# Performance work log

Measured on AMD Instinct MI355X. Metric: run time of the kernel, lower is better.

The kernel has to match this reference:

```python
import jax, jax.numpy as jnp
import numpy as np

C, Q, R, N, S = 10, 1000, 1024, 512, 10000
ALPHA, GAMMA, DIST_W, EPS_EYE = 0.25, 2.0, 0.1, 1e-4


def setup_inputs() -> dict:
    key = jax.random.key(0)
    ks = jax.random.split(key, 8)
    box_features = jax.random.normal(ks[0], (N, R), jnp.float32)
    id_labels = jax.random.randint(ks[1], (N,), 0, C, dtype=jnp.int32)
    id_data = jax.random.normal(ks[2], (C, Q, R), jnp.float32)
    id_data_counter = jnp.full((C,), Q, dtype=jnp.int32)  # full queues -> VOS path enabled
    W_pred = jax.random.normal(ks[3], (C, R), jnp.float32) * 0.02
    b_pred = jnp.zeros((C,), jnp.float32)
    w_e = jax.random.uniform(ks[4], (C, 1), jnp.float32)  # energy_score_weights ~ U[0,1)
    dist_W1 = jax.random.normal(ks[5], (512, 1), jnp.float32) * 0.5
    dist_b1 = jnp.zeros((512,), jnp.float32)
    dist_W2 = jax.random.normal(ks[6], (1, 512), jnp.float32) * 0.05
    dist_b2 = jnp.zeros((1,), jnp.float32)
    eps = jax.random.normal(ks[7], (C, S, R), jnp.float32)  # standard-normal draws for rsample
    return dict(box_features=box_features, id_labels=id_labels, id_data=id_data,
                id_data_counter=id_data_counter, W_pred=W_pred, b_pred=b_pred, w_e=w_e,
                dist_W1=dist_W1, dist_b1=dist_b1, dist_W2=dist_W2, dist_b2=dist_b2, eps=eps)


def _bce_logits(x, y):
    # binary_cross_entropy_with_logits, elementwise
    return jnp.maximum(x, 0.0) - x * y + jnp.log1p(jnp.exp(-jnp.abs(x)))


def _queue_update(id_data, counter, labels, feats):
    # Faithful sequential per-sample queue scatter (torch Python loop) as lax.scan.
    def step(carry, inp):
        data, cnt = carry
        lab, f = inp
        c = cnt[lab]
        row = data[lab]                                            # [Q,R]
        row_set = jax.lax.dynamic_update_slice(row, f[None], (c, 0))
        row_roll = jnp.concatenate([row[1:], f[None]], axis=0)     # drop oldest, append
        full = c >= row.shape[0]
        new_row = jnp.where(full, row_roll, row_set)
        data = data.at[lab].set(new_row)
        cnt = cnt.at[lab].add(jnp.where(full, 0, 1))
        return (data, cnt), None
    (data, cnt), _ = jax.lax.scan(step, (id_data, counter), (labels, feats))
    return data, cnt


def _energy(x, w_e):
    # m + log(exp(x-m) @ relu(w_e)); all classes valid (counter > 0)
    m = jnp.max(x, axis=1, keepdims=True)
    return m + jnp.log(jnp.exp(x - m) @ jax.nn.relu(w_e))


def reference(box_features, id_labels, id_data, id_data_counter, W_pred, b_pred, w_e,
              dist_W1, dist_b1, dist_W2, dist_b2, eps):
    scores = box_features @ W_pred.T + b_pred                      # [N,C]
    # ---- classification: sigmoid focal loss (sum / num_pos) ----
    t = jax.nn.one_hot(id_labels, C, dtype=scores.dtype)
    p = jax.nn.sigmoid(scores)
    ce = _bce_logits(scores, t)
    p_t = p * t + (1.0 - p) * (1.0 - t)
    alpha_t = ALPHA * t + (1.0 - ALPHA) * (1.0 - t)
    cls_loss = jnp.sum(alpha_t * ce * (1.0 - p_t) ** GAMMA) / scores.shape[0]
    # ---- per-class queue scatter (detached features) ----
    data, _ = _queue_update(id_data, id_data_counter, id_labels,
                            jax.lax.stop_gradient(box_features))
    # ---- class Gaussians: per-class mean, shared covariance ----
    mu = jnp.mean(data, axis=1)                                    # [C,R]
    x_tilda = (data - mu[:, None, :]).reshape(-1, R)               # all classes valid (full queues)
    sigma = x_tilda.T @ x_tilda / x_tilda.shape[0] + EPS_EYE * jnp.eye(R, dtype=data.dtype)
    L = jnp.linalg.cholesky(sigma)                                 # [R,R]
    # ---- VOS: rsample 10000 per class, keep lowest-density (top-1 of -log_prob) ----
    # samples = mu + eps @ L.T ; log_prob = const - 0.5*||eps||^2, so argmin density = argmax ||eps||^2
    sq = jnp.sum(eps * eps, axis=-1)                               # [C,S]
    idx = jnp.argmax(sq, axis=-1)                                  # [C]
    eps_sel = jnp.take_along_axis(eps, idx[:, None, None], axis=1)[:, 0, :]  # [C,R]
    vos_samples = mu + eps_sel @ L.T                               # [C,R]
    scores_vos = vos_samples @ W_pred.T + b_pred                   # [C,C]
    # ---- dist loss: energy score -> tiny MLP -> BCE, weight 0.1 ----
    e_all = jnp.concatenate([_energy(scores, w_e), _energy(scores_vos, w_e)], axis=0)  # [N+C,1]
    h = jax.nn.relu(e_all @ dist_W1.T + dist_b1)
    logits = (h @ dist_W2.T + dist_b2)[:, 0]                       # [N+C]
    y = jnp.concatenate([jnp.ones((scores.shape[0],), logits.dtype),
                         jnp.zeros((C,), logits.dtype)])
    dist_loss = DIST_W * jnp.mean(_bce_logits(logits, y))
    return cls_loss, dist_loss
```

## Files before the change

kernel.cpp:

```cpp
#include <hip/hip_runtime.h>
#include <stdint.h>

#define C_ 10
#define Q_ 1000
#define R_ 1024
#define N_ 512
#define S_ 10000
#define CQ 10000
#define KP 10240

#define OFF_DT    0ULL
#define OFF_GP    20971520ULL
#define OFF_SIG   37748736ULL
#define OFF_MU    41943040ULL
#define OFF_E     41984000ULL
#define OFF_CLS   41986088ULL
#define OFF_AMAX  41986096ULL
#define OFF_KC    41986176ULL
#define OFF_GOFF  41986216ULL
#define OFF_GIDX  41986256ULL

typedef __attribute__((ext_vector_type(8))) short bf16x8;
typedef __attribute__((ext_vector_type(4))) float f32x4;

__global__ void k_prep(const int* __restrict__ labels, int* kc, int* goff, int* gidx,
                       float* mu, float* cls_accum, unsigned long long* amax) {
  __shared__ int cnt[C_];
  __shared__ int off[C_];
  int t = threadIdx.x;
  if (t < C_) cnt[t] = 0;
  __syncthreads();
  for (int i = t; i < N_; i += 256) atomicAdd(&cnt[labels[i]], 1);
  __syncthreads();
  if (t == 0) {
    int acc = 0;
    for (int c = 0; c < C_; c++) { off[c] = acc; goff[c] = acc; kc[c] = cnt[c]; acc += cnt[c]; }
    for (int i = 0; i < N_; i++) { int c = labels[i]; gidx[off[c]++] = i; }
    *cls_accum = 0.f;
  }
  if (t < C_) amax[t] = 0ULL;
  for (int i = t; i < C_ * R_; i += 256) mu[i] = 0.f;
}

__global__ __launch_bounds__(256) void k_epsmax(const float* __restrict__ eps,
                                                unsigned long long* amax) {
  int c = blockIdx.y;
  int chunk = blockIdx.x;
  int t = threadIdx.x, lane = t & 63, w = t >> 6;
  const int per = 79;
  int s0 = chunk * per;
  int s1 = min(s0 + per, S_);
  float bv = -1.f; int bs = 0;
  for (int s = s0 + w; s < s1; s += 4) {
    const float4* p = (const float4*)(eps + ((size_t)c * S_ + s) * R_);
    float acc = 0.f;
#pragma unroll
    for (int m = 0; m < 4; m++) {
      float4 v = p[lane + 64 * m];
      acc += v.x * v.x + v.y * v.y + v.z * v.z + v.w * v.w;
    }
#pragma unroll
    for (int d = 32; d > 0; d >>= 1) acc += __shfl_xor(acc, d);
    if (acc > bv) { bv = acc; bs = s; }
  }
  __shared__ float svv[4]; __shared__ int ssi[4];
  if (lane == 0) { svv[w] = bv; ssi[w] = bs; }
  __syncthreads();
  if (t == 0) {
    float m = svv[0]; int mi = ssi[0];
    for (int i = 1; i < 4; i++) if (svv[i] > m) { m = svv[i]; mi = ssi[i]; }
    if (m >= 0.f) {
      unsigned long long pk = ((unsigned long long)__float_as_uint(m) << 32) | (unsigned)mi;
      atomicMax(amax + c, pk);
    }
  }
}

__global__ void k_scores(const float* __restrict__ box, const int* __restrict__ labels,
                         const float* __restrict__ Wp, const float* __restrict__ bp,
                         const float* __restrict__ we, float* __restrict__ E,
                         float* cls_accum) {
  int i = blockIdx.x;
  int lane = threadIdx.x;
  float s[C_];
#pragma unroll
  for (int k = 0; k < C_; k++) s[k] = 0.f;
  const float* bi = box + (size_t)i * R_;
  for (int r = lane; r < R_; r += 64) {
    float x = bi[r];
#pragma unroll
    for (int k = 0; k < C_; k++) s[k] += x * Wp[k * R_ + r];
  }
#pragma unroll
  for (int k = 0; k < C_; k++) {
#pragma unroll
    for (int d = 32; d > 0; d >>= 1) s[k] += __shfl_xor(s[k], d);
  }
  if (lane == 0) {
    int lab = labels[i];
    float sc[C_]; float m = -1e30f;
#pragma unroll
    for (int k = 0; k < C_; k++) { sc[k] = s[k] + bp[k]; m = fmaxf(m, sc[k]); }
    float fsum = 0.f, esum = 0.f;
#pragma unroll
    for (int k = 0; k < C_; k++) {
      float x = sc[k];
      float tt = (k == lab) ? 1.f : 0.f;
      float p = 1.f / (1.f + expf(-x));
      float ce = fmaxf(x, 0.f) - x * tt + log1pf(expf(-fabsf(x)));
      float pt = p * tt + (1.f - p) * (1.f - tt);
      float at = 0.25f * tt + 0.75f * (1.f - tt);
      float om = 1.f - pt;
      fsum += at * ce * om * om;
      esum += expf(x - m) * fmaxf(we[k], 0.f);
    }
    atomicAdd(cls_accum, fsum);
    E[i] = m + logf(esum);
  }
}

__global__ __launch_bounds__(256) void k_convert(const float* __restrict__ idd,
                                                 const float* __restrict__ box,
                                                 const int* __restrict__ kc,
                                                 const int* __restrict__ goff,
                                                 const int* __restrict__ gidx,
                                                 uint16_t* __restrict__ Dt,
                                                 float* __restrict__ mu) {
  __shared__ const float* rowsrc[64];
  __shared__ int rcls[64];
  __shared__ float T[64][65];
  int bk = blockIdx.x;
  int br = blockIdx.y;
  int t = threadIdx.x;
  int t0 = bk * 64, r0 = br * 64;
  if (t < 64) {
    int row = t0 + t;
    const float* src = nullptr; int c = -1;
    if (row < CQ) {
      c = row / Q_;
      int q = row - c * Q_;
      int k = kc[c];
      if (q < Q_ - k) src = idd + (size_t)(c * Q_ + q + k) * R_;
      else            src = box + (size_t)gidx[goff[c] + (q - (Q_ - k))] * R_;
    }
    rowsrc[t] = src; rcls[t] = c;
  }
  __syncthreads();
  int rr = t & 63, k4 = t >> 6;
#pragma unroll
  for (int it = 0; it < 16; it++) {
    int kk = k4 + it * 4;
    const float* src = rowsrc[kk];
    T[kk][rr] = src ? src[r0 + rr] : 0.f;
  }
  __syncthreads();
  if (t < 64 && t0 < CQ) {
    int c0 = rcls[0];
    float s0 = 0.f, s1 = 0.f; int c1 = -1;
    for (int kk = 0; kk < 64; kk++) {
      int c = rcls[kk]; float v = T[kk][t];
      if (c == c0) s0 += v; else if (c >= 0) { c1 = c; s1 += v; }
    }
    atomicAdd(&mu[c0 * R_ + r0 + t], s0);
    if (c1 >= 0) atomicAdd(&mu[c1 * R_ + r0 + t], s1);
  }
  int kk2 = t & 63, r4 = t >> 6;
#pragma unroll
  for (int it = 0; it < 16; it++) {
    int rr2 = r4 + it * 4;
    float v = T[kk2][rr2];
    uint32_t u = __float_as_uint(v);
    uint32_t b = (u + 0x7fffu + ((u >> 16) & 1u)) >> 16;
    Dt[(size_t)(r0 + rr2) * KP + t0 + kk2] = (uint16_t)b;
  }
}

__global__ __launch_bounds__(256) void k_gemm(const uint16_t* __restrict__ Dt,
                                              float* __restrict__ GP) {
  __shared__ uint16_t lA[128 * 64];
  __shared__ uint16_t lB[128 * 64];
  int bi = blockIdx.x, bj = blockIdx.y, bz = blockIdx.z;
  int t = threadIdx.x;
  int lane = t & 63, w = t >> 6;
  int i0 = bi * 128, j0 = bj * 128;
  int lane16 = lane & 15, quad = lane >> 4;
  int wm = w >> 1, wn = w & 1;
  int srow = t >> 1, shalf = t & 1;
  const uint4* DU = (const uint4*)Dt;
  int kz0 = bz * 320;
  f32x4 acc[4][4];
#pragma unroll
  for (int a = 0; a < 4; a++)
#pragma unroll
    for (int b = 0; b < 4; b++) acc[a][b] = (f32x4){0.f, 0.f, 0.f, 0.f};

  for (int kt8 = 0; kt8 < 320; kt8 += 8) {
    const uint4* pa = DU + (size_t)(i0 + srow) * 1280 + kz0 + kt8 + shalf * 4;
    const uint4* pb = DU + (size_t)(j0 + srow) * 1280 + kz0 + kt8 + shalf * 4;
    uint4* la4 = (uint4*)(lA + srow * 64 + shalf * 32);
    uint4* lb4 = (uint4*)(lB + srow * 64 + shalf * 32);
#pragma unroll
    for (int u = 0; u < 4; u++) la4[u] = pa[u];
#pragma unroll
    for (int u = 0; u < 4; u++) lb4[u] = pb[u];
    __syncthreads();
#pragma unroll
    for (int ch = 0; ch < 2; ch++) {
      bf16x8 af[4], bfr[4];
#pragma unroll
      for (int mi = 0; mi < 4; mi++)
        af[mi] = *(const bf16x8*)(lA + (wm * 64 + mi * 16 + lane16) * 64 + ch * 32 + quad * 8);
#pragma unroll
      for (int ni = 0; ni < 4; ni++)
        bfr[ni] = *(const bf16x8*)(lB + (wn * 64 + ni * 16 + lane16) * 64 + ch * 32 + quad * 8);
#pragma unroll
      for (int mi = 0; mi < 4; mi++)
#pragma unroll
        for (int ni = 0; ni < 4; ni++)
          acc[mi][ni] = __builtin_amdgcn_mfma_f32_16x16x32_bf16(af[mi], bfr[ni], acc[mi][ni], 0, 0, 0);
    }
    __syncthreads();
  }
  float* gp = GP + (size_t)bz * 1048576;
#pragma unroll
  for (int mi = 0; mi < 4; mi++)
#pragma unroll
    for (int ni = 0; ni < 4; ni++) {
      int col = j0 + wn * 64 + ni * 16 + lane16;
      int rowb = i0 + wm * 64 + mi * 16 + quad * 4;
#pragma unroll
      for (int r = 0; r < 4; r++)
        gp[(size_t)(rowb + r) * 1024 + col] = acc[mi][ni][r];
    }
}

__global__ void k_reduce(const float* __restrict__ GP, const float* __restrict__ mu,
                         float* __restrict__ sig) {
  int idx = blockIdx.x * 256 + threadIdx.x;
  int i = idx >> 10, j = idx & 1023;
  float g = GP[idx] + GP[idx + 1048576] + GP[idx + 2097152] + GP[idx + 3145728];
  float mm = 0.f;
#pragma unroll
  for (int c = 0; c < C_; c++) mm += mu[c * R_ + i] * mu[c * R_ + j];
  sig[idx] = g * 1e-4f - mm * 1e-7f + ((i == j) ? 1e-4f : 0.f);
}

#define AIDX(i, j) (((i) << 7) + (((j) + (i)) & 127))
__global__ __launch_bounds__(256) void k_chol_diag(float* __restrict__ sig, int p) {
  __shared__ float a[16384];
  int t = threadIdx.x;
  int base = p * 128;
  int lane = t & 63, wv = t >> 6;
  for (int idx = t; idx < 16384; idx += 256) {
    int i = idx >> 7, j = idx & 127;
    a[AIDX(i, j)] = sig[(size_t)(base + i) * 1024 + base + j];
  }
  __syncthreads();
  for (int panel = 0; panel < 8; panel++) {
    int j0 = panel * 16;
    if (wv == 0) {
      float pa0[16], pa1[16];
#pragma unroll
      for (int jj = 0; jj < 16; jj++) {
        pa0[jj] = a[AIDX(lane, j0 + jj)];
        pa1[jj] = a[AIDX(lane + 64, j0 + jj)];
      }
#pragma unroll
      for (int jj = 0; jj < 16; jj++) {
        int j = j0 + jj;
        float pv0 = __shfl(pa0[jj], j & 63);
        float pv1 = __shfl(pa1[jj], j & 63);
        float pv = (j < 64) ? pv0 : pv1;
        float rsq = rsqrtf(pv);
        rsq = rsq * (1.5f - 0.5f * pv * rsq * rsq);
        pa0[jj] *= rsq;
        pa1[jj] *= rsq;
#pragma unroll
        for (int kk = jj + 1; kk < 16; kk++) {
          int k = j0 + kk;
          float av0 = __shfl(pa0[jj], k & 63);
          float av1 = __shfl(pa1[jj], k & 63);
          float akj = (k < 64) ? av0 : av1;
          pa0[kk] -= pa0[jj] * akj;
          pa1[kk] -= pa1[jj] * akj;
        }
      }
#pragma unroll
      for (int jj = 0; jj < 16; jj++) {
        a[AIDX(lane, j0 + jj)] = pa0[jj];
        a[AIDX(lane + 64, j0 + jj)] = pa1[jj];
      }
    }
    __syncthreads();
    int m0 = j0 + 16;
    int M = 128 - m0;
    if (M > 0) {
      int T4 = M >> 2;
      int ntiles = T4 * (T4 + 1) / 2;
      for (int tb = t; tb < ntiles; tb += 256) {
        int I = (int)((sqrtf(8.f * tb + 1.f) - 1.f) * 0.5f);
        while ((I + 1) * (I + 2) / 2 <= tb) I++;
        while (I * (I + 1) / 2 > tb) I--;
        int K = tb - I * (I + 1) / 2;
        int gi = m0 + I * 4, gk = m0 + K * 4;
        float acc[4][4] = {{0.f}};
#pragma unroll
        for (int u = 0; u < 16; u++) {
          int jj = (u + t) & 15;
          float ai[4], ak[4];
#pragma unroll
          for (int m = 0; m < 4; m++) ai[m] = a[AIDX(gi + m, j0 + jj)];
#pragma unroll
          for (int n = 0; n < 4; n++) ak[n] = a[AIDX(gk + n, j0 + jj)];
#pragma unroll
          for (int m = 0; m < 4; m++)
#pragma unroll
            for (int n = 0; n < 4; n++) acc[m][n] += ai[m] * ak[n];
        }
#pragma unroll
        for (int m = 0; m < 4; m++)
#pragma unroll
          for (int n = 0; n < 4; n++)
            a[AIDX(gi + m, gk + n)] -= acc[m][n];
      }
    }
    __syncthreads();
  }
  for (int idx = t; idx < 16384; idx += 256) {
    int i = idx >> 7, j = idx & 127;
    sig[(size_t)(base + i) * 1024 + base + j] = a[AIDX(i, j)];
  }
}

#define XIDX(j, r) (((j) << 6) + (((r) + (j)) & 63))
__global__ __launch_bounds__(256) void k_chol_trsm(float* __restrict__ sig, int p) {
  __shared__ float Ls[8128];
  __shared__ float XT[8192];
  int t = threadIdx.x;
  int base = p * 128;
  int row0 = base + 128 + blockIdx.x * 64;
  int r = t & 63, wv = t >> 6;
  for (int idx = t; idx < 8128; idx += 256) {
    int k = (int)((sqrtf(8.f * idx + 1.f) + 1.f) * 0.5f);
    while (k * (k - 1) / 2 > idx) k--;
    while ((k + 1) * k / 2 <= idx) k++;
    int j = idx - k * (k - 1) / 2;
    Ls[idx] = sig[(size_t)(base + k) * 1024 + base + j];
  }
  for (int idx = t; idx < 8192; idx += 256) {
    int rr = idx >> 7, j = idx & 127;
    XT[XIDX(j, rr)] = sig[(size_t)(row0 + rr) * 1024 + base + j];
  }
  float rd0 = 0.f, rd1 = 0.f;
  if (wv == 0) {
    rd0 = 1.0f / sig[(size_t)(base + r) * 1024 + base + r];
    rd1 = 1.0f / sig[(size_t)(base + 64 + r) * 1024 + base + 64 + r];
  }
  __syncthreads();
  for (int pb = 0; pb < 8; pb++) {
    int j0 = pb * 16;
    if (j0 > 0) {
      int c0 = j0 + wv * 4;
      int b0 = c0 * (c0 - 1) / 2, b1 = (c0 + 1) * c0 / 2;
      int b2 = (c0 + 2) * (c0 + 1) / 2, b3 = (c0 + 3) * (c0 + 2) / 2;
      float acc0 = 0.f, acc1 = 0.f, acc2 = 0.f, acc3 = 0.f;
      for (int k = 0; k < j0; k++) {
        float xk = XT[XIDX(k, r)];
        acc0 += xk * Ls[b0 + k];
        acc1 += xk * Ls[b1 + k];
        acc2 += xk * Ls[b2 + k];
        acc3 += xk * Ls[b3 + k];
      }
      XT[XIDX(c0 + 0, r)] -= acc0;
      XT[XIDX(c0 + 1, r)] -= acc1;
      XT[XIDX(c0 + 2, r)] -= acc2;
      XT[XIDX(c0 + 3, r)] -= acc3;
    }
    __syncthreads();
    if (wv == 0) {
#pragma unroll
      for (int jj = 0; jj < 16; jj++) {
        int j = j0 + jj;
        float rdj = (j < 64) ? __shfl(rd0, j & 63) : __shfl(rd1, j & 63);
        float xj = XT[XIDX(j, r)] * rdj;
        XT[XIDX(j, r)] = xj;
#pragma unroll
        for (int kk = jj + 1; kk < 16; kk++) {
          int k2 = j0 + kk;
          XT[XIDX(k2, r)] -= xj * Ls[k2 * (k2 - 1) / 2 + j];
        }
      }
    }
    __syncthreads();
  }
  for (int idx = t; idx < 8192; idx += 256) {
    int rr = idx >> 7, j = idx & 127;
    sig[(size_t)(row0 + rr) * 1024 + base + j] = XT[XIDX(j, rr)];
  }
}

__global__ __launch_bounds__(256) void k_chol_syrk(float* __restrict__ sig, int p) {
  __shared__ float PA[64][65], PB[64][65];
  int t = threadIdx.x;
  int tb = p * 128 + 128;
  int bx = blockIdx.x;
  int I = 0;
  while ((I + 1) * (I + 2) / 2 <= bx) I++;
  int K = bx - I * (I + 1) / 2;
  int gi = tb + I * 64, gk = tb + K * 64;
  int a4 = t >> 4, b4 = t & 15;
  float acc[4][4];
#pragma unroll
  for (int m = 0; m < 4; m++)
#pragma unroll
    for (int n = 0; n < 4; n++) acc[m][n] = 0.f;
  for (int ch = 0; ch < 2; ch++) {
    int cb = p * 128 + ch * 64;
    for (int idx = t; idx < 4096; idx += 256) {
      int rr = idx >> 6, cc = idx & 63;
      PA[rr][cc] = sig[(size_t)(gi + rr) * 1024 + cb + cc];
      PB[rr][cc] = sig[(size_t)(gk + rr) * 1024 + cb + cc];
    }
    __syncthreads();
    for (int j = 0; j < 64; j++) {
      float pa[4], pb[4];
#pragma unroll
      for (int m = 0; m < 4; m++) pa[m] = PA[a4 * 4 + m][j];
#pragma unroll
      for (int n = 0; n < 4; n++) pb[n] = PB[b4 * 4 + n][j];
#pragma unroll
      for (int m = 0; m < 4; m++)
#pragma unroll
        for (int n = 0; n < 4; n++) acc[m][n] += pa[m] * pb[n];
    }
    __syncthreads();
  }
#pragma unroll
  for (int m = 0; m < 4; m++)
#pragma unroll
    for (int n = 0; n < 4; n++)
      sig[(size_t)(gi + a4 * 4 + m) * 1024 + gk + b4 * 4 + n] -= acc[m][n];
}

__global__ __launch_bounds__(256) void k_vos(const float* __restrict__ eps,
                                             const float* __restrict__ L,
                                             const float* __restrict__ mu,
                                             const float* __restrict__ Wp,
                                             const float* __restrict__ bp,
                                             const float* __restrict__ we,
                                             const unsigned long long* __restrict__ amax,
                                             float* __restrict__ E) {
  __shared__ float es[1024];
  __shared__ float ys[1024];
  __shared__ float sv[16];
  int c = blockIdx.x, t = threadIdx.x;
  int idx = (int)(amax[c] & 0xffffffffULL);
  for (int i = t; i < 1024; i += 256) es[i] = eps[((size_t)c * S_ + idx) * R_ + i];
  __syncthreads();
  for (int rep = 0; rep < 4; rep++) {
    int i = rep * 256 + t;
    const float* Lr = L + (size_t)i * 1024;
    float a0 = 0.f, a1 = 0.f, a2 = 0.f, a3 = 0.f;
    int j = 0;
    for (; j + 3 <= i; j += 4) {
      a0 += es[j] * Lr[j];
      a1 += es[j + 1] * Lr[j + 1];
      a2 += es[j + 2] * Lr[j + 2];
      a3 += es[j + 3] * Lr[j + 3];
    }
    for (; j <= i; j++) a0 += es[j] * Lr[j];
    ys[i] = mu[c * R_ + i] * 1e-3f + ((a0 + a1) + (a2 + a3));
  }
  __syncthreads();
  if (t < C_) {
    float acc = bp[t];
    const float* Wr = Wp + (size_t)t * R_;
    for (int j = 0; j < 1024; j++) acc += ys[j] * Wr[j];
    sv[t] = acc;
  }
  __syncthreads();
  if (t == 0) {
    float m = -1e30f;
    for (int k = 0; k < C_; k++) m = fmaxf(m, sv[k]);
    float sum = 0.f;
    for (int k = 0; k < C_; k++) sum += expf(sv[k] - m) * fmaxf(we[k], 0.f);
    E[N_ + c] = m + logf(sum);
  }
}

__global__ __launch_bounds__(256) void k_dist(const float* __restrict__ E,
                                              const float* __restrict__ W1,
                                              const float* __restrict__ b1,
                                              const float* __restrict__ W2,
                                              const float* __restrict__ b2,
                                              const float* __restrict__ cls_accum,
                                              float* __restrict__ out) {
  __shared__ float sW1[512], sb1[512], sW2[512];
  __shared__ float red[4];
  int t = threadIdx.x;
  for (int i = t; i < 512; i += 256) { sW1[i] = W1[i]; sb1[i] = b1[i]; sW2[i] = W2[i]; }
  __syncthreads();
  float sum = 0.f;
  for (int i = t; i < N_ + C_; i += 256) {
    float e = E[i];
    float acc = b2[0];
    for (int j = 0; j < 512; j++) acc += sW2[j] * fmaxf(e * sW1[j] + sb1[j], 0.f);
    float y = (i < N_) ? 1.f : 0.f;
    float l = fmaxf(acc, 0.f) - acc * y + log1pf(expf(-fabsf(acc)));
    sum += l;
  }
#pragma unroll
  for (int d = 32; d > 0; d >>= 1) sum += __shfl_xor(sum, d);
  if ((t & 63) == 0) red[t >> 6] = sum;
  __syncthreads();
  if (t == 0) {
    out[1] = 0.1f * (red[0] + red[1] + red[2] + red[3]) / 522.f;
    out[0] = *cls_accum / 512.f;
  }
}

extern "C" void kernel_launch(void* const* d_in, const int* in_sizes, int n_in,
                              void* d_out, int out_size, void* d_ws, size_t ws_size,
                              hipStream_t stream) {
  (void)in_sizes; (void)n_in; (void)out_size; (void)ws_size;
  const float* box  = (const float*)d_in[0];
  const int*   lab  = (const int*)d_in[1];
  const float* idd  = (const float*)d_in[2];
  const float* Wp   = (const float*)d_in[4];
  const float* bp   = (const float*)d_in[5];
  const float* we   = (const float*)d_in[6];
  const float* W1   = (const float*)d_in[7];
  const float* b1   = (const float*)d_in[8];
  const float* W2   = (const float*)d_in[9];
  const float* b2   = (const float*)d_in[10];
  const float* eps  = (const float*)d_in[11];
  float* out = (float*)d_out;

  char* ws = (char*)d_ws;
  uint16_t* Dt = (uint16_t*)(ws + OFF_DT);
  float* GP    = (float*)(ws + OFF_GP);
  float* sig   = (float*)(ws + OFF_SIG);
  float* mu    = (float*)(ws + OFF_MU);
  float* E     = (float*)(ws + OFF_E);
  float* clsa  = (float*)(ws + OFF_CLS);
  unsigned long long* amax = (unsigned long long*)(ws + OFF_AMAX);
  int* kc   = (int*)(ws + OFF_KC);
  int* goff = (int*)(ws + OFF_GOFF);
  int* gidx = (int*)(ws + OFF_GIDX);

  hipLaunchKernelGGL(k_prep, dim3(1), dim3(256), 0, stream, lab, kc, goff, gidx, mu, clsa, amax);
  hipLaunchKernelGGL(k_epsmax, dim3(127, C_), dim3(256), 0, stream, eps, amax);
  hipLaunchKernelGGL(k_scores, dim3(N_), dim3(64), 0, stream, box, lab, Wp, bp, we, E, clsa);
  hipLaunchKernelGGL(k_convert, dim3(160, 16), dim3(256), 0, stream, idd, box, kc, goff, gidx, Dt, mu);
  hipLaunchKernelGGL(k_gemm, dim3(8, 8, 4), dim3(256), 0, stream, Dt, GP);
  hipLaunchKernelGGL(k_reduce, dim3(4096), dim3(256), 0, stream, GP, mu, sig);
  for (int p = 0; p < 8; p++) {
    hipLaunchKernelGGL(k_chol_diag, dim3(1), dim3(256), 0, stream, sig, p);
    int rows = 1024 - 128 * (p + 1);
    if (rows > 0) {
      int nb = rows / 64;
      hipLaunchKernelGGL(k_chol_trsm, dim3(nb), dim3(256), 0, stream, sig, p);
      hipLaunchKernelGGL(k_chol_syrk, dim3(nb * (nb + 1) / 2), dim3(256), 0, stream, sig, p);
    }
  }
  hipLaunchKernelGGL(k_vos, dim3(C_), dim3(256), 0, stream, eps, sig, mu, Wp, bp, we, amax, E);
  hipLaunchKernelGGL(k_dist, dim3(1), dim3(256), 0, stream, E, W1, b1, W2, b2, clsa, out);
}
```

Baseline: 2.023 ms.

## Fuse Cholesky stages into cooperative kernel; double-buffer and swizzle split-K GEMM

The 23 separate Cholesky, VOS and dist launches become one cooperative kernel with 105 blocks that steps through the panels using grid.sync, which removes per-launch overhead and gaps between kernels. The Gram GEMM now uses register-staged double-buffered LDS with an XOR swizzle to avoid bank conflicts. Split-K rises from 4 to 8 so more blocks are in flight, at the cost of a larger partial-sum buffer and more reduction reads. Grid syncs on a single stream add their own latency, and correctness depends on all 105 blocks being co-resident.

```diff
diff --git a/kernel.cpp b/kernel.cpp
--- a/kernel.cpp
+++ b/kernel.cpp
@@ -1,5 +1,8 @@
 #include <hip/hip_runtime.h>
+#include <hip/hip_cooperative_groups.h>
 #include <stdint.h>
+
+namespace cg = cooperative_groups;
 
 #define C_ 10
 #define Q_ 1000
@@ -8,17 +11,19 @@
 #define S_ 10000
 #define CQ 10000
 #define KP 10240
+#define SPLITK 8
+#define GRIDC 105
 
 #define OFF_DT    0ULL
 #define OFF_GP    20971520ULL
-#define OFF_SIG   37748736ULL
-#define OFF_MU    41943040ULL
-#define OFF_E     41984000ULL
-#define OFF_CLS   41986088ULL
-#define OFF_AMAX  41986096ULL
-#define OFF_KC    41986176ULL
-#define OFF_GOFF  41986216ULL
-#define OFF_GIDX  41986256ULL
+#define OFF_SIG   54525952ULL
+#define OFF_MU    58720256ULL
+#define OFF_E     58761216ULL
+#define OFF_CLS   58763304ULL
+#define OFF_AMAX  58763312ULL
+#define OFF_KC    58763392ULL
+#define OFF_GOFF  58763432ULL
+#define OFF_GIDX  58763472ULL
 
 typedef __attribute__((ext_vector_type(8))) short bf16x8;
 typedef __attribute__((ext_vector_type(4))) float f32x4;
@@ -177,47 +182,82 @@
 
 __global__ __launch_bounds__(256) void k_gemm(const uint16_t* __restrict__ Dt,
                                               float* __restrict__ GP) {
-  __shared__ uint16_t lA[128 * 64];
-  __shared__ uint16_t lB[128 * 64];
+  __shared__ __align__(16) uint16_t lA[2][8192];
+  __shared__ __align__(16) uint16_t lB[2][8192];
   int bi = blockIdx.x, bj = blockIdx.y, bz = blockIdx.z;
   int t = threadIdx.x;
   int lane = t & 63, w = t >> 6;
   int i0 = bi * 128, j0 = bj * 128;
   int lane16 = lane & 15, quad = lane >> 4;
   int wm = w >> 1, wn = w & 1;
-  int srow = t >> 1, shalf = t & 1;
-  const uint4* DU = (const uint4*)Dt;
-  int kz0 = bz * 320;
+  int row = t >> 1, half = t & 1;
+  int kz = bz * 1280;
+  const uint16_t* ga = Dt + (size_t)(i0 + row) * KP + kz + half * 32;
+  const uint16_t* gb = Dt + (size_t)(j0 + row) * KP + kz + half * 32;
+  int swz[4];
+#pragma unroll
+  for (int u = 0; u < 4; u++) swz[u] = (((half << 2) | u) ^ (row & 7)) << 3;
+  int x7 = lane16 & 7;
+
   f32x4 acc[4][4];
 #pragma unroll
   for (int a = 0; a < 4; a++)
 #pragma unroll
     for (int b = 0; b < 4; b++) acc[a][b] = (f32x4){0.f, 0.f, 0.f, 0.f};
 
-  for (int kt8 = 0; kt8 < 320; kt8 += 8) {
-    const uint4* pa = DU + (size_t)(i0 + srow) * 1280 + kz0 + kt8 + shalf * 4;
-    const uint4* pb = DU + (size_t)(j0 + srow) * 1280 + kz0 + kt8 + shalf * 4;
-    uint4* la4 = (uint4*)(lA + srow * 64 + shalf * 32);
-    uint4* lb4 = (uint4*)(lB + srow * 64 + shalf * 32);
-#pragma unroll
-    for (int u = 0; u < 4; u++) la4[u] = pa[u];
-#pragma unroll
-    for (int u = 0; u < 4; u++) lb4[u] = pb[u];
-    __syncthreads();
+  uint4 ra[4], rb[4];
+#pragma unroll
+  for (int u = 0; u < 4; u++) {
+    ra[u] = *(const uint4*)(ga + u * 8);
+    rb[u] = *(const uint4*)(gb + u * 8);
+  }
+#pragma unroll
+  for (int u = 0; u < 4; u++) {
+    *(uint4*)(lA[0] + row * 64 + swz[u]) = ra[u];
+    *(uint4*)(lB[0] + row * 64 + swz[u]) = rb[u];
+  }
+  __syncthreads();
+
+  for (int it = 0; it < 20; it++) {
+    int cur = it & 1;
+    bool more = (it + 1) < 20;
+    if (more) {
+      const uint16_t* pa = ga + (it + 1) * 64;
+      const uint16_t* pb = gb + (it + 1) * 64;
+#pragma unroll
+      for (int u = 0; u < 4; u++) {
+        ra[u] = *(const uint4*)(pa + u * 8);
+        rb[u] = *(const uint4*)(pb + u * 8);
+      }
+    }
 #pragma unroll
     for (int ch = 0; ch < 2; ch++) {
       bf16x8 af[4], bfr[4];
 #pragma unroll
-      for (int mi = 0; mi < 4; mi++)
-        af[mi] = *(const bf16x8*)(lA + (wm * 64 + mi * 16 + lane16) * 64 + ch * 32 + quad * 8);
-#pragma unroll
-      for (int ni = 0; ni < 4; ni++)
-        bfr[ni] = *(const bf16x8*)(lB + (wn * 64 + ni * 16 + lane16) * 64 + ch * 32 + quad * 8);
+      for (int mi = 0; mi < 4; mi++) {
+        int r = wm * 64 + mi * 16 + lane16;
+        int ck = ((ch << 2) | quad) ^ x7;
+        af[mi] = *(const bf16x8*)(lA[cur] + r * 64 + ck * 8);
+      }
+#pragma unroll
+      for (int ni = 0; ni < 4; ni++) {
+        int r = wn * 64 + ni * 16 + lane16;
+        int ck = ((ch << 2) | quad) ^ x7;
+        bfr[ni] = *(const bf16x8*)(lB[cur] + r * 64 + ck * 8);
+      }
 #pragma unroll
       for (int mi = 0; mi < 4; mi++)
 #pragma unroll
         for (int ni = 0; ni < 4; ni++)
           acc[mi][ni] = __builtin_amdgcn_mfma_f32_16x16x32_bf16(af[mi], bfr[ni], acc[mi][ni], 0, 0, 0);
+    }
+    if (more) {
+      int nxt = cur ^ 1;
+#pragma unroll
+      for (int u = 0; u < 4; u++) {
+        *(uint4*)(lA[nxt] + row * 64 + swz[u]) = ra[u];
+        *(uint4*)(lB[nxt] + row * 64 + swz[u]) = rb[u];
+      }
     }
     __syncthreads();
   }
@@ -238,7 +278,9 @@
                          float* __restrict__ sig) {
   int idx = blockIdx.x * 256 + threadIdx.x;
   int i = idx >> 10, j = idx & 1023;
-  float g = GP[idx] + GP[idx + 1048576] + GP[idx + 2097152] + GP[idx + 3145728];
+  float g = 0.f;
+#pragma unroll
+  for (int s2 = 0; s2 < SPLITK; s2++) g += GP[idx + s2 * 1048576];
   float mm = 0.f;
 #pragma unroll
   for (int c = 0; c < C_; c++) mm += mu[c * R_ + i] * mu[c * R_ + j];
@@ -246,8 +288,7 @@
 }
 
 #define AIDX(i, j) (((i) << 7) + (((j) + (i)) & 127))
-__global__ __launch_bounds__(256) void k_chol_diag(float* __restrict__ sig, int p) {
-  __shared__ float a[16384];
+__device__ void chol_diag_body(float* __restrict__ sig, int p, float* __restrict__ a) {
   int t = threadIdx.x;
   int base = p * 128;
   int lane = t & 63, wv = t >> 6;
@@ -333,12 +374,12 @@
 }
 
 #define XIDX(j, r) (((j) << 6) + (((r) + (j)) & 63))
-__global__ __launch_bounds__(256) void k_chol_trsm(float* __restrict__ sig, int p) {
-  __shared__ float Ls[8128];
-  __shared__ float XT[8192];
+__device__ void chol_trsm_body(float* __restrict__ sig, int p, int bid, float* __restrict__ smem) {
+  float* Ls = smem;
+  float* XT = smem + 8192;
   int t = threadIdx.x;
   int base = p * 128;
-  int row0 = base + 128 + blockIdx.x * 64;
+  int row0 = base + 128 + bid * 64;
   int r = t & 63, wv = t >> 6;
   for (int idx = t; idx < 8128; idx += 256) {
     int k = (int)((sqrtf(8.f * idx + 1.f) + 1.f) * 0.5f);
@@ -399,14 +440,14 @@
   }
 }
 
-__global__ __launch_bounds__(256) void k_chol_syrk(float* __restrict__ sig, int p) {
-  __shared__ float PA[64][65], PB[64][65];
+__device__ void chol_syrk_body(float* __restrict__ sig, int p, int bid, float* __restrict__ smem) {
+  float (*PA)[65] = (float(*)[65])smem;
+  float (*PB)[65] = (float(*)[65])(smem + 4160);
   int t = threadIdx.x;
   int tb = p * 128 + 128;
-  int bx = blockIdx.x;
   int I = 0;
-  while ((I + 1) * (I + 2) / 2 <= bx) I++;
-  int K = bx - I * (I + 1) / 2;
+  while ((I + 1) * (I + 2) / 2 <= bid) I++;
+  int K = bid - I * (I + 1) / 2;
   int gi = tb + I * 64, gk = tb + K * 64;
   int a4 = t >> 4, b4 = t & 15;
   float acc[4][4];
@@ -442,18 +483,15 @@
       sig[(size_t)(gi + a4 * 4 + m) * 1024 + gk + b4 * 4 + n] -= acc[m][n];
 }
 
-__global__ __launch_bounds__(256) void k_vos(const float* __restrict__ eps,
-                                             const float* __restrict__ L,
-                                             const float* __restrict__ mu,
-                                             const float* __restrict__ Wp,
-                                             const float* __restrict__ bp,
-                                             const float* __restrict__ we,
-                                             const unsigned long long* __restrict__ amax,
-                                             float* __restrict__ E) {
-  __shared__ float es[1024];
-  __shared__ float ys[1024];
-  __shared__ float sv[16];
-  int c = blockIdx.x, t = threadIdx.x;
+__device__ void vos_body(const float* __restrict__ eps, const float* __restrict__ L,
+                         const float* __restrict__ mu, const float* __restrict__ Wp,
+                         const float* __restrict__ bp, const float* __restrict__ we,
+                         const unsigned long long* __restrict__ amax,
+                         float* __restrict__ E, int c, float* __restrict__ smem) {
+  float* es = smem;
+  float* ys = smem + 1024;
+  float* sv = smem + 2048;
+  int t = threadIdx.x;
   int idx = (int)(amax[c] & 0xffffffffULL);
   for (int i = t; i < 1024; i += 256) es[i] = eps[((size_t)c * S_ + idx) * R_ + i];
   __syncthreads();
@@ -488,15 +526,14 @@
   }
 }
 
-__global__ __launch_bounds__(256) void k_dist(const float* __restrict__ E,
-                                              const float* __restrict__ W1,
-                                              const float* __restrict__ b1,
-                                              const float* __restrict__ W2,
-                                              const float* __restrict__ b2,
-                                              const float* __restrict__ cls_accum,
-                                              float* __restrict__ out) {
-  __shared__ float sW1[512], sb1[512], sW2[512];
-  __shared__ float red[4];
+__device__ void dist_body(const float* __restrict__ E, const float* __restrict__ W1,
+                          const float* __restrict__ b1, const float* __restrict__ W2,
+                          const float* __restrict__ b2, const float* __restrict__ cls_accum,
+                          float* __restrict__ out, float* __restrict__ smem) {
+  float* sW1 = smem;
+  float* sb1 = smem + 512;
+  float* sW2 = smem + 1024;
+  float* red = smem + 1536;
   int t = threadIdx.x;
   for (int i = t; i < 512; i += 256) { sW1[i] = W1[i]; sb1[i] = b1[i]; sW2[i] = W2[i]; }
   __syncthreads();
@@ -517,6 +554,34 @@
     out[1] = 0.1f * (red[0] + red[1] + red[2] + red[3]) / 522.f;
     out[0] = *cls_accum / 512.f;
   }
+}
+
+__global__ __launch_bounds__(256) void k_chol(float* __restrict__ sig,
+    const float* __restrict__ eps, const float* __restrict__ mu,
+    const float* __restrict__ Wp, const float* __restrict__ bp,
+    const float* __restrict__ we, const unsigned long long* __restrict__ amax,
+    float* __restrict__ E, const float* __restrict__ W1, const float* __restrict__ b1,
+    const float* __restrict__ W2, const float* __restrict__ b2,
+    const float* __restrict__ cls_accum, float* __restrict__ out) {
+  cg::grid_group grid = cg::this_grid();
+  __shared__ __align__(16) float smem[16384];
+  int bid = blockIdx.x;
+  for (int p = 0; p < 8; p++) {
+    if (bid == 0) chol_diag_body(sig, p, smem);
+    __threadfence(); grid.sync();
+    int rows = 1024 - 128 * (p + 1);
+    if (rows > 0) {
+      int nb = rows >> 6;
+      if (bid < nb) chol_trsm_body(sig, p, bid, smem);
+      __threadfence(); grid.sync();
+      int nt = nb * (nb + 1) / 2;
+      for (int bx = bid; bx < nt; bx += GRIDC) chol_syrk_body(sig, p, bx, smem);
+      __threadfence(); grid.sync();
+    }
+  }
+  if (bid < C_) vos_body(eps, sig, mu, Wp, bp, we, amax, E, bid, smem);
+  __threadfence(); grid.sync();
+  if (bid == 0) dist_body(E, W1, b1, W2, b2, cls_accum, out, smem);
 }
 
 extern "C" void kernel_launch(void* const* d_in, const int* in_sizes, int n_in,
@@ -552,17 +617,14 @@
   hipLaunchKernelGGL(k_epsmax, dim3(127, C_), dim3(256), 0, stream, eps, amax);
   hipLaunchKernelGGL(k_scores, dim3(N_), dim3(64), 0, stream, box, lab, Wp, bp, we, E, clsa);
   hipLaunchKernelGGL(k_convert, dim3(160, 16), dim3(256), 0, stream, idd, box, kc, goff, gidx, Dt, mu);
-  hipLaunchKernelGGL(k_gemm, dim3(8, 8, 4), dim3(256), 0, stream, Dt, GP);
+  hipLaunchKernelGGL(k_gemm, dim3(8, 8, SPLITK), dim3(256), 0, stream, Dt, GP);
   hipLaunchKernelGGL(k_reduce, dim3(4096), dim3(256), 0, stream, GP, mu, sig);
-  for (int p = 0; p < 8; p++) {
-    hipLaunchKernelGGL(k_chol_diag, dim3(1), dim3(256), 0, stream, sig, p);
-    int rows = 1024 - 128 * (p + 1);
-    if (rows > 0) {
-      int nb = rows / 64;
-      hipLaunchKernelGGL(k_chol_trsm, dim3(nb), dim3(256), 0, stream, sig, p);
-      hipLaunchKernelGGL(k_chol_syrk, dim3(nb * (nb + 1) / 2), dim3(256), 0, stream, sig, p);
-    }
-  }
-  hipLaunchKernelGGL(k_vos, dim3(C_), dim3(256), 0, stream, eps, sig, mu, Wp, bp, we, amax, E);
-  hipLaunchKernelGGL(k_dist, dim3(1), dim3(256), 0, stream, E, W1, b1, W2, b2, clsa, out);
-}
+  {
+    float* a0 = sig; const float* a1 = eps; const float* a2 = mu; const float* a3 = Wp;
+    const float* a4 = bp; const float* a5 = we; const unsigned long long* a6 = amax;
+    float* a7 = E; const float* a8 = W1; const float* a9 = b1; const float* a10 = W2;
+    const float* a11 = b2; const float* a12 = clsa; float* a13 = out;
+    void* args[] = {&a0, &a1, &a2, &a3, &a4, &a5, &a6, &a7, &a8, &a9, &a10, &a11, &a12, &a13};
+    hipLaunchCooperativeKernel(k_chol, dim3(GRIDC), dim3(256), args, 0, stream);
+  }
+}
```

After: 2.515 ms. +24.3%, slower.
